# Kernel optimization log

Measured on AMD Instinct MI355X. Metric: run time of the kernel, lower is better.

The kernel has to match this reference:

```python
import jax, jax.numpy as jnp
import numpy as np

WINDOW = 4
TEMP = 0.01
WIDTH = 256
EPS = 1e-12


def _l2norm(x, axis):
    n = jnp.sqrt(jnp.sum(x * x, axis=axis, keepdims=True))
    return x / jnp.maximum(n, EPS)


def _src_coords():
    # torch.meshgrid default = 'ij': v varies over rows, u over cols; coords = (u, v)
    v, u = jnp.meshgrid(jnp.arange(WIDTH, dtype=jnp.float32),
                        jnp.arange(WIDTH, dtype=jnp.float32), indexing='ij')
    return jnp.stack((u.reshape(-1), v.reshape(-1)), axis=1)  # (HW, 2)


def setup_inputs() -> dict:
    key = jax.random.key(0)
    k1, k2, k3, k4 = jax.random.split(key, 4)
    BW, S, C, N = 8, 1, 64, 256
    return {
        'keypoint_scores': jax.random.uniform(k1, (BW, S, N), dtype=jnp.float32),
        'keypoint_desc': jax.random.normal(k2, (BW, C, N), dtype=jnp.float32),
        'desc_dense': jax.random.normal(k3, (BW, C, WIDTH, WIDTH), dtype=jnp.float32),
        'keypoint_coords': jax.random.uniform(k4, (BW, N, 2), dtype=jnp.float32) * (WIDTH - 1),
    }


def reference(keypoint_scores, keypoint_desc, desc_dense, keypoint_coords):
    BW, C, N = keypoint_desc.shape
    B = BW // WINDOW
    HW = WIDTH * WIDTH

    # source = first frame of each window; normalize descriptors over channel dim
    src = desc_dense[::WINDOW].reshape(B, C, HW)            # (B, C, HW)
    src = _l2norm(src, axis=1)
    tgt = keypoint_desc.reshape(B, WINDOW, C, N)[:, 1:]     # (B, w-1, C, N)
    tgt = _l2norm(tgt, axis=2)

    # cosine similarity -> temperature softmax over dense source pixels
    match = jnp.einsum('bwcn,bcm->bwnm', tgt, src) / TEMP   # (B, w-1, N, HW)
    soft = jax.nn.softmax(match, axis=-1)

    coords = _src_coords()                                   # (HW, 2)
    pseudo = jnp.einsum('bwnm,md->bwnd', soft, coords)       # (B, w-1, N, 2)
    pseudo_coords = pseudo.reshape(B * (WINDOW - 1), N, 2)

    base = jnp.arange(B, dtype=jnp.int64) * WINDOW
    tgt_ids = (base[:, None] + jnp.arange(1, WINDOW, dtype=jnp.int64)[None, :]).reshape(-1)
    src_ids = jnp.repeat(base, WINDOW - 1)

    return (pseudo_coords, keypoint_scores[tgt_ids], tgt_ids, src_ids)
```

## Files before the change

kernel.cpp:

```cpp
#include <hip/hip_runtime.h>
#include <hip/hip_bf16.h>

typedef _Float16 h8_t __attribute__((ext_vector_type(8)));
typedef float f4_t __attribute__((ext_vector_type(4)));

#define HWPX 65536

__global__ __launch_bounds__(256) void k_pix(
    const float* __restrict__ dense, _Float16* __restrict__ Kn)
{
    int gid = blockIdx.x * 256 + threadIdx.x;
    int pid = gid >> 1;
    int h = gid & 1;
    int b = pid >> 16, m = pid & 65535;
    const float* src = dense + ((size_t)(b * 4) * 64 + h * 32) * HWPX + m;
    float v[32];
    float ss = 0.f;
#pragma unroll
    for (int c = 0; c < 32; ++c) { float x = src[(size_t)c * HWPX]; v[c] = x; ss += x * x; }
    ss += __shfl_xor(ss, 1, 64);
    float inv = 1.0f / fmaxf(sqrtf(ss), 1e-12f);
    h8_t* dst = (h8_t*)(Kn + (size_t)pid * 64 + h * 32);
#pragma unroll
    for (int i = 0; i < 4; ++i) {
        h8_t hv;
#pragma unroll
        for (int j = 0; j < 8; ++j) hv[j] = (_Float16)(v[i * 8 + j] * inv);
        dst[i] = hv;
    }
}

__global__ __launch_bounds__(256) void k_kp(
    const float* __restrict__ kdesc, _Float16* __restrict__ Qn)
{
    int q = blockIdx.x * 256 + threadIdx.x;
    int b = q / 768;
    int w = (q >> 8) % 3;
    int n = q & 255;
    int frame = b * 4 + 1 + w;
    const float* src = kdesc + (size_t)frame * 64 * 256 + n;
    float v[64]; float ss = 0.f;
#pragma unroll
    for (int c = 0; c < 64; ++c) { float x = src[c * 256]; v[c] = x; ss += x * x; }
    float inv = 1.0f / fmaxf(sqrtf(ss), 1e-12f);
    h8_t* dst = (h8_t*)(Qn + (size_t)q * 64);
#pragma unroll
    for (int i = 0; i < 8; ++i) {
        h8_t hv;
#pragma unroll
        for (int j = 0; j < 8; ++j) hv[j] = (_Float16)(v[i * 8 + j] * inv);
        dst[i] = hv;
    }
}

__global__ __launch_bounds__(256) void k_attn(
    const _Float16* __restrict__ Qn, const _Float16* __restrict__ Kn,
    float* __restrict__ partials)
{
    int tid = threadIdx.x;
    int seg = blockIdx.x;
    int qg = blockIdx.y, b = blockIdx.z;
    int qbase = b * 768 + qg * 256;
    int lane = tid & 63, wave = tid >> 6;
    int col = lane & 15, quad = lane >> 4;

    h8_t af[4][2];
    const _Float16* qrow = Qn + (size_t)(qbase + wave * 64 + col) * 64 + quad * 8;
#pragma unroll
    for (int qt = 0; qt < 4; ++qt)
#pragma unroll
        for (int ks = 0; ks < 2; ++ks)
            af[qt][ks] = *(const h8_t*)(qrow + qt * 16 * 64 + ks * 32);

    float l[4][4], sb[4][4], sv[4][4];
#pragma unroll
    for (int qt = 0; qt < 4; ++qt)
#pragma unroll
        for (int r = 0; r < 4; ++r) { l[qt][r] = 0.f; sb[qt][r] = 0.f; sv[qt][r] = 0.f; }

    const _Float16* Kg = Kn + ((size_t)b * HWPX + seg * 1024) * 64 + quad * 8;

    h8_t b0 = *(const h8_t*)(Kg + col * 64);
    h8_t b1 = *(const h8_t*)(Kg + col * 64 + 32);

#pragma unroll 4
    for (int nt = 0; nt < 64; ++nt) {
        h8_t n0, n1;
        if (nt < 63) {
            const _Float16* p = Kg + ((nt + 1) * 16 + col) * 64;
            n0 = *(const h8_t*)(p);
            n1 = *(const h8_t*)(p + 32);
        }
        f4_t acc[4];
#pragma unroll
        for (int qt = 0; qt < 4; ++qt) {
            f4_t z = {0.f, 0.f, 0.f, 0.f};
            acc[qt] = __builtin_amdgcn_mfma_f32_16x16x32_f16(af[qt][0], b0, z, 0, 0, 0);
        }
#pragma unroll
        for (int qt = 0; qt < 4; ++qt)
            acc[qt] = __builtin_amdgcn_mfma_f32_16x16x32_f16(af[qt][1], b1, acc[qt], 0, 0, 0);

        float ubase = (float)((nt & 15) * 16);
        float vf = (float)(seg * 4 + (nt >> 4));
#pragma unroll
        for (int qt = 0; qt < 4; ++qt)
#pragma unroll
            for (int r = 0; r < 4; ++r) {
                float w = exp2f(fmaf(acc[qt][r], 144.26950408889634f, -144.26950408889634f));
                l[qt][r] += w;
                sb[qt][r] = fmaf(w, ubase, sb[qt][r]);
                sv[qt][r] = fmaf(w, vf, sv[qt][r]);
            }
        b0 = n0; b1 = n1;
    }

    float colf = (float)col;
#pragma unroll
    for (int qt = 0; qt < 4; ++qt)
#pragma unroll
        for (int r = 0; r < 4; ++r) {
            float a = l[qt][r];
            float x = fmaf(colf, a, sb[qt][r]);
            float y = sv[qt][r];
#pragma unroll
            for (int m = 1; m < 16; m <<= 1) {
                a += __shfl_xor(a, m, 64);
                x += __shfl_xor(x, m, 64);
                y += __shfl_xor(y, m, 64);
            }
            if (col == 0) {
                int q = qbase + wave * 64 + qt * 16 + quad * 4 + r;
                partials[(q * 3 + 0) * 64 + seg] = a;
                partials[(q * 3 + 1) * 64 + seg] = x;
                partials[(q * 3 + 2) * 64 + seg] = y;
            }
        }
}

__global__ __launch_bounds__(256) void k_final(
    const float* __restrict__ partials, const float* __restrict__ kscores,
    float* __restrict__ out, int out_size)
{
    int idx = blockIdx.x * 256 + threadIdx.x;
    if (idx >= out_size) return;
    if (idx < 3072) {
        int q = idx >> 1;
        const float* pl = partials + (q * 3 + 0) * 64;
        const float* ps = partials + (q * 3 + 1 + (idx & 1)) * 64;
        float l = 0.f, s = 0.f;
#pragma unroll
        for (int i = 0; i < 64; ++i) { l += pl[i]; s += ps[i]; }
        out[idx] = s / l;
    } else if (idx < 4608) {
        int i = idx - 3072;
        int j = i >> 8, n = i & 255;
        int frame = j + 1 + (j / 3);
        out[idx] = kscores[frame * 256 + n];
    } else if (idx < 4620) {
        int i = idx - 4608;
        if (i < 6) out[idx] = (float)(i + 1 + i / 3);
        else { int j = i - 6; out[idx] = (float)((j / 3) * 4); }
    }
}

extern "C" void kernel_launch(void* const* d_in, const int* in_sizes, int n_in,
                              void* d_out, int out_size, void* d_ws, size_t ws_size,
                              hipStream_t stream) {
    const float* kp_scores = (const float*)d_in[0];
    const float* kp_desc   = (const float*)d_in[1];
    const float* dense     = (const float*)d_in[2];

    _Float16* Qn = (_Float16*)d_ws;
    _Float16* Kn = (_Float16*)((char*)d_ws + 196608);
    float* partials = (float*)((char*)d_ws + 196608 + 16777216);

    hipLaunchKernelGGL(k_pix, dim3(1024), dim3(256), 0, stream, dense, Kn);
    hipLaunchKernelGGL(k_kp, dim3(6), dim3(256), 0, stream, kp_desc, Qn);
    hipLaunchKernelGGL(k_attn, dim3(64, 3, 2), dim3(256), 0, stream,
                       Qn, Kn, partials);
    hipLaunchKernelGGL(k_final, dim3(19), dim3(256), 0, stream,
                       partials, kp_scores, (float*)d_out, out_size);
}
```

Before: 241.2 us.

## Merge preprocessing kernels, double attention segments, hoist row-coordinate accumulation

Fuses the pixel and keypoint normalization kernels into a single launch. It also doubles the number of attention segments from 64 to 128, so each block handles 512 pixels and the grid has more blocks to spread across the CUs. The per-element v-coordinate FMA becomes a per-row update based on the difference in the running sum of l. The trade-offs are more partials for the final reduction to sum and a little extra register use for lprev.

```diff
diff --git a/kernel.cpp b/kernel.cpp
--- a/kernel.cpp
+++ b/kernel.cpp
@@ -5,51 +5,51 @@
 typedef float f4_t __attribute__((ext_vector_type(4)));
 
 #define HWPX 65536
+#define SEGS 128
 
-__global__ __launch_bounds__(256) void k_pix(
-    const float* __restrict__ dense, _Float16* __restrict__ Kn)
+__global__ __launch_bounds__(256) void k_pre(
+    const float* __restrict__ dense, const float* __restrict__ kdesc,
+    _Float16* __restrict__ Qn, _Float16* __restrict__ Kn)
 {
-    int gid = blockIdx.x * 256 + threadIdx.x;
-    int pid = gid >> 1;
-    int h = gid & 1;
-    int b = pid >> 16, m = pid & 65535;
-    const float* src = dense + ((size_t)(b * 4) * 64 + h * 32) * HWPX + m;
-    float v[32];
-    float ss = 0.f;
+    int bid = blockIdx.x, tid = threadIdx.x;
+    if (bid < 1024) {
+        int gid = bid * 256 + tid;
+        int pid = gid >> 1, h = gid & 1;
+        int b = pid >> 16, m = pid & 65535;
+        const float* src = dense + ((size_t)(b * 4) * 64 + h * 32) * HWPX + m;
+        float v[32];
+        float ss = 0.f;
 #pragma unroll
-    for (int c = 0; c < 32; ++c) { float x = src[(size_t)c * HWPX]; v[c] = x; ss += x * x; }
-    ss += __shfl_xor(ss, 1, 64);
-    float inv = 1.0f / fmaxf(sqrtf(ss), 1e-12f);
-    h8_t* dst = (h8_t*)(Kn + (size_t)pid * 64 + h * 32);
+        for (int c = 0; c < 32; ++c) { float x = src[(size_t)c * HWPX]; v[c] = x; ss += x * x; }
+        ss += __shfl_xor(ss, 1, 64);
+        float inv = 1.0f / fmaxf(sqrtf(ss), 1e-12f);
+        h8_t* dst = (h8_t*)(Kn + (size_t)pid * 64 + h * 32);
 #pragma unroll
-    for (int i = 0; i < 4; ++i) {
-        h8_t hv;
+        for (int i = 0; i < 4; ++i) {
+            h8_t hv;
 #pragma unroll
-        for (int j = 0; j < 8; ++j) hv[j] = (_Float16)(v[i * 8 + j] * inv);
-        dst[i] = hv;
-    }
-}
-
-__global__ __launch_bounds__(256) void k_kp(
-    const float* __restrict__ kdesc, _Float16* __restrict__ Qn)
-{
-    int q = blockIdx.x * 256 + threadIdx.x;
-    int b = q / 768;
-    int w = (q >> 8) % 3;
-    int n = q & 255;
-    int frame = b * 4 + 1 + w;
-    const float* src = kdesc + (size_t)frame * 64 * 256 + n;
-    float v[64]; float ss = 0.f;
+            for (int j = 0; j < 8; ++j) hv[j] = (_Float16)(v[i * 8 + j] * inv);
+            dst[i] = hv;
+        }
+    } else {
+        int q = (bid - 1024) * 256 + tid;
+        int b = q / 768;
+        int w = (q >> 8) % 3;
+        int n = q & 255;
+        int frame = b * 4 + 1 + w;
+        const float* src = kdesc + (size_t)frame * 64 * 256 + n;
+        float v[64]; float ss = 0.f;
 #pragma unroll
-    for (int c = 0; c < 64; ++c) { float x = src[c * 256]; v[c] = x; ss += x * x; }
-    float inv = 1.0f / fmaxf(sqrtf(ss), 1e-12f);
-    h8_t* dst = (h8_t*)(Qn + (size_t)q * 64);
+        for (int c = 0; c < 64; ++c) { float x = src[c * 256]; v[c] = x; ss += x * x; }
+        float inv = 1.0f / fmaxf(sqrtf(ss), 1e-12f);
+        h8_t* dst = (h8_t*)(Qn + (size_t)q * 64);
 #pragma unroll
-    for (int i = 0; i < 8; ++i) {
-        h8_t hv;
+        for (int i = 0; i < 8; ++i) {
+            h8_t hv;
 #pragma unroll
-        for (int j = 0; j < 8; ++j) hv[j] = (_Float16)(v[i * 8 + j] * inv);
-        dst[i] = hv;
+            for (int j = 0; j < 8; ++j) hv[j] = (_Float16)(v[i * 8 + j] * inv);
+            dst[i] = hv;
+        }
     }
 }
 
@@ -72,47 +72,57 @@
         for (int ks = 0; ks < 2; ++ks)
             af[qt][ks] = *(const h8_t*)(qrow + qt * 16 * 64 + ks * 32);
 
-    float l[4][4], sb[4][4], sv[4][4];
+    float l[4][4], sb[4][4], sv[4][4], lprev[4][4];
 #pragma unroll
     for (int qt = 0; qt < 4; ++qt)
 #pragma unroll
-        for (int r = 0; r < 4; ++r) { l[qt][r] = 0.f; sb[qt][r] = 0.f; sv[qt][r] = 0.f; }
+        for (int r = 0; r < 4; ++r) { l[qt][r] = 0.f; sb[qt][r] = 0.f; sv[qt][r] = 0.f; lprev[qt][r] = 0.f; }
 
-    const _Float16* Kg = Kn + ((size_t)b * HWPX + seg * 1024) * 64 + quad * 8;
+    const _Float16* Kg = Kn + ((size_t)b * HWPX + seg * 512) * 64 + quad * 8;
 
     h8_t b0 = *(const h8_t*)(Kg + col * 64);
     h8_t b1 = *(const h8_t*)(Kg + col * 64 + 32);
 
+#pragma unroll
+    for (int g = 0; g < 2; ++g) {
 #pragma unroll 4
-    for (int nt = 0; nt < 64; ++nt) {
-        h8_t n0, n1;
-        if (nt < 63) {
-            const _Float16* p = Kg + ((nt + 1) * 16 + col) * 64;
-            n0 = *(const h8_t*)(p);
-            n1 = *(const h8_t*)(p + 32);
+        for (int t = 0; t < 16; ++t) {
+            int nt = g * 16 + t;
+            h8_t n0, n1;
+            if (nt < 31) {
+                const _Float16* p = Kg + ((nt + 1) * 16 + col) * 64;
+                n0 = *(const h8_t*)(p);
+                n1 = *(const h8_t*)(p + 32);
+            }
+            f4_t acc[4];
+#pragma unroll
+            for (int qt = 0; qt < 4; ++qt) {
+                f4_t z = {0.f, 0.f, 0.f, 0.f};
+                acc[qt] = __builtin_amdgcn_mfma_f32_16x16x32_f16(af[qt][0], b0, z, 0, 0, 0);
+            }
+#pragma unroll
+            for (int qt = 0; qt < 4; ++qt)
+                acc[qt] = __builtin_amdgcn_mfma_f32_16x16x32_f16(af[qt][1], b1, acc[qt], 0, 0, 0);
+
+            float ubase = (float)(t * 16);
+#pragma unroll
+            for (int qt = 0; qt < 4; ++qt)
+#pragma unroll
+                for (int r = 0; r < 4; ++r) {
+                    float w = exp2f(fmaf(acc[qt][r], 144.26950408889634f, -144.26950408889634f));
+                    l[qt][r] += w;
+                    sb[qt][r] = fmaf(w, ubase, sb[qt][r]);
+                }
+            b0 = n0; b1 = n1;
         }
-        f4_t acc[4];
-#pragma unroll
-        for (int qt = 0; qt < 4; ++qt) {
-            f4_t z = {0.f, 0.f, 0.f, 0.f};
-            acc[qt] = __builtin_amdgcn_mfma_f32_16x16x32_f16(af[qt][0], b0, z, 0, 0, 0);
-        }
-#pragma unroll
-        for (int qt = 0; qt < 4; ++qt)
-            acc[qt] = __builtin_amdgcn_mfma_f32_16x16x32_f16(af[qt][1], b1, acc[qt], 0, 0, 0);
-
-        float ubase = (float)((nt & 15) * 16);
-        float vf = (float)(seg * 4 + (nt >> 4));
+        float vf = (float)(seg * 2 + g);
 #pragma unroll
         for (int qt = 0; qt < 4; ++qt)
 #pragma unroll
             for (int r = 0; r < 4; ++r) {
-                float w = exp2f(fmaf(acc[qt][r], 144.26950408889634f, -144.26950408889634f));
-                l[qt][r] += w;
-                sb[qt][r] = fmaf(w, ubase, sb[qt][r]);
-                sv[qt][r] = fmaf(w, vf, sv[qt][r]);
+                sv[qt][r] = fmaf(vf, l[qt][r] - lprev[qt][r], sv[qt][r]);
+                lprev[qt][r] = l[qt][r];
             }
-        b0 = n0; b1 = n1;
     }
 
     float colf = (float)col;
@@ -131,9 +141,9 @@
             }
             if (col == 0) {
                 int q = qbase + wave * 64 + qt * 16 + quad * 4 + r;
-                partials[(q * 3 + 0) * 64 + seg] = a;
-                partials[(q * 3 + 1) * 64 + seg] = x;
-                partials[(q * 3 + 2) * 64 + seg] = y;
+                partials[(q * 3 + 0) * SEGS + seg] = a;
+                partials[(q * 3 + 1) * SEGS + seg] = x;
+                partials[(q * 3 + 2) * SEGS + seg] = y;
             }
         }
 }
@@ -146,11 +156,11 @@
     if (idx >= out_size) return;
     if (idx < 3072) {
         int q = idx >> 1;
-        const float* pl = partials + (q * 3 + 0) * 64;
-        const float* ps = partials + (q * 3 + 1 + (idx & 1)) * 64;
+        const float* pl = partials + (q * 3 + 0) * SEGS;
+        const float* ps = partials + (q * 3 + 1 + (idx & 1)) * SEGS;
         float l = 0.f, s = 0.f;
-#pragma unroll
-        for (int i = 0; i < 64; ++i) { l += pl[i]; s += ps[i]; }
+#pragma unroll 8
+        for (int i = 0; i < SEGS; ++i) { l += pl[i]; s += ps[i]; }
         out[idx] = s / l;
     } else if (idx < 4608) {
         int i = idx - 3072;
@@ -175,10 +185,8 @@
     _Float16* Kn = (_Float16*)((char*)d_ws + 196608);
     float* partials = (float*)((char*)d_ws + 196608 + 16777216);
 
-    hipLaunchKernelGGL(k_pix, dim3(1024), dim3(256), 0, stream, dense, Kn);
-    hipLaunchKernelGGL(k_kp, dim3(6), dim3(256), 0, stream, kp_desc, Qn);
-    hipLaunchKernelGGL(k_attn, dim3(64, 3, 2), dim3(256), 0, stream,
-                       Qn, Kn, partials);
+    hipLaunchKernelGGL(k_pre, dim3(1030), dim3(256), 0, stream, dense, kp_desc, Qn, Kn);
+    hipLaunchKernelGGL(k_attn, dim3(SEGS, 3, 2), dim3(256), 0, stream, Qn, Kn, partials);
     hipLaunchKernelGGL(k_final, dim3(19), dim3(256), 0, stream,
                        partials, kp_scores, (float*)d_out, out_size);
 }
```

New measurement: 232.1 us. -3.8%, faster.
